# Optimization experiments

Measured on AMD Instinct MI355X. Metric: run time of the kernel, lower is better.

The kernel has to match this reference:

```python
import jax, jax.numpy as jnp
import numpy as np

H = 32  # hidden size per direction (hard-wired in module)


def _gru_scan(x_proj, W_hh, b_hh, reverse):
    """x_proj: [T, B, 3H] = x @ W_ih.T + b_ih (precomputed). Returns all hidden states [T, B, H].
    Gate order follows PyTorch: (r, z, n)."""
    def step(h, xp):
        gh = h @ W_hh.T + b_hh                      # [B, 3H]
        xr, xz, xn = jnp.split(xp, 3, axis=-1)
        hr, hz, hn = jnp.split(gh, 3, axis=-1)
        r = jax.nn.sigmoid(xr + hr)
        z = jax.nn.sigmoid(xz + hz)
        n = jnp.tanh(xn + r * hn)
        h_new = (1.0 - z) * n + z * h
        return h_new, h_new

    B = x_proj.shape[1]
    h0 = jnp.zeros((B, H), x_proj.dtype)
    _, ys = jax.lax.scan(step, h0, x_proj, reverse=reverse)
    return ys  # ys[t] = hidden after consuming x[t] (fwd) or x[T-1..t] (bwd)


def setup_inputs() -> dict:
    key = jax.random.key(0)
    ks = jax.random.split(key, 14)
    B, T = 2048, 512
    s_ih = 1.0 / np.sqrt(H)
    inp = {
        "x": jax.random.normal(ks[0], (B, T, 1), dtype=jnp.float32),
        # forward-direction GRU params (PyTorch layout: [3H, in], [3H, H], [3H])
        "W_ih_f": jax.random.uniform(ks[1], (3 * H, 1), jnp.float32, -s_ih, s_ih),
        "W_hh_f": jax.random.uniform(ks[2], (3 * H, H), jnp.float32, -s_ih, s_ih),
        "b_ih_f": jax.random.uniform(ks[3], (3 * H,), jnp.float32, -s_ih, s_ih),
        "b_hh_f": jax.random.uniform(ks[4], (3 * H,), jnp.float32, -s_ih, s_ih),
        # backward-direction GRU params
        "W_ih_b": jax.random.uniform(ks[5], (3 * H, 1), jnp.float32, -s_ih, s_ih),
        "W_hh_b": jax.random.uniform(ks[6], (3 * H, H), jnp.float32, -s_ih, s_ih),
        "b_ih_b": jax.random.uniform(ks[7], (3 * H,), jnp.float32, -s_ih, s_ih),
        "b_hh_b": jax.random.uniform(ks[8], (3 * H,), jnp.float32, -s_ih, s_ih),
        # MLP head: Linear(64,16) -> ReLU -> Linear(16,1) -> Sigmoid
        "W1": jax.random.uniform(ks[9], (16, 2 * H), jnp.float32, -0.125, 0.125),
        "b1": jax.random.uniform(ks[10], (16,), jnp.float32, -0.125, 0.125),
        "W2": jax.random.uniform(ks[11], (1, 16), jnp.float32, -0.25, 0.25),
        "b2": jax.random.uniform(ks[12], (1,), jnp.float32, -0.25, 0.25),
    }
    return inp


def reference(x, W_ih_f, W_hh_f, b_ih_f, b_hh_f,
              W_ih_b, W_hh_b, b_ih_b, b_hh_b,
              W1, b1, W2, b2):
    xt = jnp.swapaxes(x, 0, 1)                 # [T, B, 1]
    # Precompute input projections for all timesteps (input_size=1 so this is cheap)
    xpf = xt @ W_ih_f.T + b_ih_f               # [T, B, 3H]
    xpb = xt @ W_ih_b.T + b_ih_b               # [T, B, 3H]
    ys_f = _gru_scan(xpf, W_hh_f, b_hh_f, reverse=False)
    ys_b = _gru_scan(xpb, W_hh_b, b_hh_b, reverse=True)
    # out[:, -1, :] in torch = concat(fwd hidden at t=T-1, bwd hidden at t=T-1)
    out_last = jnp.concatenate([ys_f[-1], ys_b[-1]], axis=-1)   # [B, 64]
    h1 = jax.nn.relu(out_last @ W1.T + b1)                      # [B, 16]
    return jax.nn.sigmoid(h1 @ W2.T + b2)                       # [B, 1]
```

## Files before the change

### kernel.cpp

```cpp
#include <hip/hip_runtime.h>


typedef float vf2 __attribute__((ext_vector_type(2)));
typedef float vf4 __attribute__((ext_vector_type(4)));
typedef _Float16 f16;
typedef f16 h2 __attribute__((ext_vector_type(2)));
typedef f16 h8 __attribute__((ext_vector_type(8)));

#define TT 512
#define HH 32

#define PIN(v) asm volatile("" : "+v"(v))

#define LOG2E 1.44269504f

__device__ __forceinline__ float fast_sigm(float a) {
  return __builtin_amdgcn_rcpf(1.0f + __builtin_amdgcn_exp2f(-LOG2E * a));
}
__device__ __forceinline__ float fast_tanh(float a) {
  return __builtin_fmaf(-2.0f,
      __builtin_amdgcn_rcpf(1.0f + __builtin_amdgcn_exp2f(2.0f * LOG2E * a)),
      1.0f);
}

__device__ __forceinline__ h2 pack_h2(vf2 a, float s) {
  h2 r = {(f16)(a.x * s), (f16)(a.y * s)};
  return r;
}

#define LDW16(P, BASE, S) \
  h2 P##0=pack_h2(Wp[(BASE)+0],(S)),  P##1=pack_h2(Wp[(BASE)+1],(S)), \
     P##2=pack_h2(Wp[(BASE)+2],(S)),  P##3=pack_h2(Wp[(BASE)+3],(S)), \
     P##4=pack_h2(Wp[(BASE)+4],(S)),  P##5=pack_h2(Wp[(BASE)+5],(S)), \
     P##6=pack_h2(Wp[(BASE)+6],(S)),  P##7=pack_h2(Wp[(BASE)+7],(S)), \
     P##8=pack_h2(Wp[(BASE)+8],(S)),  P##9=pack_h2(Wp[(BASE)+9],(S)), \
     P##A=pack_h2(Wp[(BASE)+10],(S)), P##B=pack_h2(Wp[(BASE)+11],(S)), \
     P##C=pack_h2(Wp[(BASE)+12],(S)), P##D=pack_h2(Wp[(BASE)+13],(S)), \
     P##E=pack_h2(Wp[(BASE)+14],(S)), P##F=pack_h2(Wp[(BASE)+15],(S)); \
  PIN(P##0);PIN(P##1);PIN(P##2);PIN(P##3);PIN(P##4);PIN(P##5);PIN(P##6);PIN(P##7); \
  PIN(P##8);PIN(P##9);PIN(P##A);PIN(P##B);PIN(P##C);PIN(P##D);PIN(P##E);PIN(P##F)

#define FDOT16(A0, A1, P, SEED) \
  float A0 = __builtin_amdgcn_fdot2(q0, P##0, (SEED), false); \
  float A1 = __builtin_amdgcn_fdot2(q1, P##1, 0.0f, false); \
  A0 = __builtin_amdgcn_fdot2(q2, P##2, A0, false);  A1 = __builtin_amdgcn_fdot2(q3, P##3, A1, false); \
  A0 = __builtin_amdgcn_fdot2(q4, P##4, A0, false);  A1 = __builtin_amdgcn_fdot2(q5, P##5, A1, false); \
  A0 = __builtin_amdgcn_fdot2(q6, P##6, A0, false);  A1 = __builtin_amdgcn_fdot2(q7, P##7, A1, false); \
  A0 = __builtin_amdgcn_fdot2(q8, P##8, A0, false);  A1 = __builtin_amdgcn_fdot2(q9, P##9, A1, false); \
  A0 = __builtin_amdgcn_fdot2(qA, P##A, A0, false);  A1 = __builtin_amdgcn_fdot2(qB, P##B, A1, false); \
  A0 = __builtin_amdgcn_fdot2(qC, P##C, A0, false);  A1 = __builtin_amdgcn_fdot2(qD, P##D, A1, false); \
  A0 = __builtin_amdgcn_fdot2(qE, P##E, A0, false);  A1 = __builtin_amdgcn_fdot2(qF, P##F, A1, false)

__global__ __launch_bounds__(256)
__attribute__((amdgpu_waves_per_eu(1, 1)))
void gru_bidir_head(const float* __restrict__ X,
                    const float* __restrict__ Wih_f, const float* __restrict__ Whh_f,
                    const float* __restrict__ bih_f, const float* __restrict__ bhh_f,
                    const float* __restrict__ Wih_b,
                    const float* __restrict__ bih_b, const float* __restrict__ bhh_b,
                    const float* __restrict__ W1, const float* __restrict__ b1,
                    const float* __restrict__ W2, const float* __restrict__ b2,
                    float* __restrict__ out)
{
  __shared__ float xbuf[8][TT];
  __shared__ f16   hbuf[8][HH];
  __shared__ float obuf[8][64];

  const int g  = threadIdx.x & 31;
  const int rs = threadIdx.x >> 5;
  const int b  = (blockIdx.x << 3) + rs;

  const vf4* Xr4 = (const vf4*)(X + (size_t)b * TT);
  vf4* xb4 = (vf4*)&xbuf[rs][0];
  #pragma unroll
  for (int q = 0; q < 4; ++q) xb4[g + 32 * q] = Xr4[g + 32 * q];

  const vf2* Wp = (const vf2*)Whh_f;
  const float s1 = -LOG2E;
  const float s2 = 2.0f * LOG2E;
  LDW16(Wr, g * 16, s1);
  LDW16(Wz, (HH + g) * 16, s1);
  LDW16(Wn, (2 * HH + g) * 16, s2);

  float xwr = Wih_f[g] * s1, xwz = Wih_f[HH + g] * s1, xwn = Wih_f[2*HH + g] * s2;
  float cbr = (bih_f[g]      + bhh_f[g])      * s1;
  float cbz = (bih_f[HH + g] + bhh_f[HH + g]) * s1;
  float cbn = bih_f[2*HH + g] * s2;
  float cbh = bhh_f[2*HH + g] * s2;
  PIN(xwr); PIN(xwz); PIN(xwn); PIN(cbr); PIN(cbz); PIN(cbn); PIN(cbh);

  float h = 0.0f;
  hbuf[rs][g] = (f16)0.0f;
  __builtin_amdgcn_wave_barrier();

  const h8*  hv = (const h8*)&hbuf[rs][0];
  const vf4* xv = (const vf4*)&xbuf[rs][0];
  vf4 x4 = xv[0];

  #pragma unroll 1
  for (int tg = 0; tg < TT / 4; ++tg) {
    const vf4 x4n = xv[tg + 1 < TT / 4 ? tg + 1 : tg];
    #pragma unroll
    for (int u = 0; u < 4; ++u) {
      const float x = (u == 0) ? x4.x : (u == 1) ? x4.y : (u == 2) ? x4.z : x4.w;

      h8 H0 = hv[0], H1 = hv[1], H2 = hv[2], H3 = hv[3];
      h2 q0 = {H0[0], H0[1]}, q1 = {H0[2], H0[3]}, q2 = {H0[4], H0[5]}, q3 = {H0[6], H0[7]},
         q4 = {H1[0], H1[1]}, q5 = {H1[2], H1[3]}, q6 = {H1[4], H1[5]}, q7 = {H1[6], H1[7]},
         q8 = {H2[0], H2[1]}, q9 = {H2[2], H2[3]}, qA = {H2[4], H2[5]}, qB = {H2[6], H2[7]},
         qC = {H3[0], H3[1]}, qD = {H3[2], H3[3]}, qE = {H3[4], H3[5]}, qF = {H3[6], H3[7]};
      asm volatile("" : "+v"(q0), "+v"(q1), "+v"(q2), "+v"(q3),
                        "+v"(q4), "+v"(q5), "+v"(q6), "+v"(q7),
                        "+v"(q8), "+v"(q9), "+v"(qA), "+v"(qB),
                        "+v"(qC), "+v"(qD), "+v"(qE), "+v"(qF));

      FDOT16(Ra, Rb, Wr, __builtin_fmaf(x, xwr, cbr));
      FDOT16(Za, Zb, Wz, __builtin_fmaf(x, xwz, cbz));
      FDOT16(Na, Nb, Wn, cbh);

      const float ar = Ra + Rb;
      const float az = Za + Zb;
      const float r = __builtin_amdgcn_rcpf(1.0f + __builtin_amdgcn_exp2f(ar));
      const float z = __builtin_amdgcn_rcpf(1.0f + __builtin_amdgcn_exp2f(az));
      const float y = __builtin_fmaf(r, Na + Nb, __builtin_fmaf(x, xwn, cbn));
      const float n = __builtin_fmaf(-2.0f,
          __builtin_amdgcn_rcpf(1.0f + __builtin_amdgcn_exp2f(y)), 1.0f);
      h = __builtin_fmaf(z, h - n, n);

      hbuf[rs][g] = (f16)h;
      __builtin_amdgcn_wave_barrier();
    }
    x4 = x4n;
  }

  const float xl  = xbuf[rs][TT - 1];
  const float rb  = fast_sigm(__builtin_fmaf(xl, Wih_b[g],      bih_b[g]      + bhh_b[g]));
  const float zb  = fast_sigm(__builtin_fmaf(xl, Wih_b[HH + g], bih_b[HH + g] + bhh_b[HH + g]));
  const float xnb = __builtin_fmaf(xl, Wih_b[2*HH + g], bih_b[2*HH + g]);
  const float nb  = fast_tanh(__builtin_fmaf(rb, bhh_b[2*HH + g], xnb));
  const float hb  = nb - zb * nb;

  obuf[rs][g]      = h;
  obuf[rs][32 + g] = hb;
  __builtin_amdgcn_wave_barrier();

  const int j = g & 15;
  const vf4* W1r = (const vf4*)(W1 + j * 64);
  const vf4* hc  = (const vf4*)&obuf[rs][0];
  vf4 a4 = W1r[0] * hc[0];
  #pragma unroll
  for (int q = 1; q < 16; ++q)
    a4 = __builtin_elementwise_fma(W1r[q], hc[q], a4);
  float acc = b1[j] + (a4.x + a4.y) + (a4.z + a4.w);
  float h1 = fmaxf(acc, 0.0f) * W2[j];
  h1 += __shfl_down(h1, 8, 16);
  h1 += __shfl_down(h1, 4, 16);
  h1 += __shfl_down(h1, 2, 16);
  h1 += __shfl_down(h1, 1, 16);
  if (g == 0) out[b] = fast_sigm(h1 + b2[0]);
}

extern "C" void kernel_launch(void* const* d_in, const int* in_sizes, int n_in,
                              void* d_out, int out_size, void* d_ws, size_t ws_size,
                              hipStream_t stream) {
  const float* X     = (const float*)d_in[0];
  const float* Wih_f = (const float*)d_in[1];
  const float* Whh_f = (const float*)d_in[2];
  const float* bih_f = (const float*)d_in[3];
  const float* bhh_f = (const float*)d_in[4];
  const float* Wih_b = (const float*)d_in[5];
  const float* bih_b = (const float*)d_in[7];
  const float* bhh_b = (const float*)d_in[8];
  const float* W1    = (const float*)d_in[9];
  const float* b1    = (const float*)d_in[10];
  const float* W2    = (const float*)d_in[11];
  const float* b2    = (const float*)d_in[12];
  float* out = (float*)d_out;

  gru_bidir_head<<<256, 256, 0, stream>>>(X, Wih_f, Whh_f, bih_f, bhh_f,
                                          Wih_b, bih_b, bhh_b, W1, b1, W2, b2, out);
}
```

Measured before the change: 177.4 us.

## Split GRU hidden-dot reduction across wave halves, one batch row per wave

```diff
diff --git a/kernel.cpp b/kernel.cpp
--- a/kernel.cpp
+++ b/kernel.cpp
@@ -28,31 +28,27 @@
   return r;
 }
 
-#define LDW16(P, BASE, S) \
-  h2 P##0=pack_h2(Wp[(BASE)+0],(S)),  P##1=pack_h2(Wp[(BASE)+1],(S)), \
-     P##2=pack_h2(Wp[(BASE)+2],(S)),  P##3=pack_h2(Wp[(BASE)+3],(S)), \
-     P##4=pack_h2(Wp[(BASE)+4],(S)),  P##5=pack_h2(Wp[(BASE)+5],(S)), \
-     P##6=pack_h2(Wp[(BASE)+6],(S)),  P##7=pack_h2(Wp[(BASE)+7],(S)), \
-     P##8=pack_h2(Wp[(BASE)+8],(S)),  P##9=pack_h2(Wp[(BASE)+9],(S)), \
-     P##A=pack_h2(Wp[(BASE)+10],(S)), P##B=pack_h2(Wp[(BASE)+11],(S)), \
-     P##C=pack_h2(Wp[(BASE)+12],(S)), P##D=pack_h2(Wp[(BASE)+13],(S)), \
-     P##E=pack_h2(Wp[(BASE)+14],(S)), P##F=pack_h2(Wp[(BASE)+15],(S)); \
-  PIN(P##0);PIN(P##1);PIN(P##2);PIN(P##3);PIN(P##4);PIN(P##5);PIN(P##6);PIN(P##7); \
-  PIN(P##8);PIN(P##9);PIN(P##A);PIN(P##B);PIN(P##C);PIN(P##D);PIN(P##E);PIN(P##F)
+#define LDW8(P, BASE, S) \
+  h2 P##0=pack_h2(Wp[(BASE)+0],(S)), P##1=pack_h2(Wp[(BASE)+1],(S)), \
+     P##2=pack_h2(Wp[(BASE)+2],(S)), P##3=pack_h2(Wp[(BASE)+3],(S)), \
+     P##4=pack_h2(Wp[(BASE)+4],(S)), P##5=pack_h2(Wp[(BASE)+5],(S)), \
+     P##6=pack_h2(Wp[(BASE)+6],(S)), P##7=pack_h2(Wp[(BASE)+7],(S)); \
+  PIN(P##0);PIN(P##1);PIN(P##2);PIN(P##3);PIN(P##4);PIN(P##5);PIN(P##6);PIN(P##7)
 
-#define FDOT16(A0, A1, P, SEED) \
-  float A0 = __builtin_amdgcn_fdot2(q0, P##0, (SEED), false); \
-  float A1 = __builtin_amdgcn_fdot2(q1, P##1, 0.0f, false); \
-  A0 = __builtin_amdgcn_fdot2(q2, P##2, A0, false);  A1 = __builtin_amdgcn_fdot2(q3, P##3, A1, false); \
-  A0 = __builtin_amdgcn_fdot2(q4, P##4, A0, false);  A1 = __builtin_amdgcn_fdot2(q5, P##5, A1, false); \
-  A0 = __builtin_amdgcn_fdot2(q6, P##6, A0, false);  A1 = __builtin_amdgcn_fdot2(q7, P##7, A1, false); \
-  A0 = __builtin_amdgcn_fdot2(q8, P##8, A0, false);  A1 = __builtin_amdgcn_fdot2(q9, P##9, A1, false); \
-  A0 = __builtin_amdgcn_fdot2(qA, P##A, A0, false);  A1 = __builtin_amdgcn_fdot2(qB, P##B, A1, false); \
-  A0 = __builtin_amdgcn_fdot2(qC, P##C, A0, false);  A1 = __builtin_amdgcn_fdot2(qD, P##D, A1, false); \
-  A0 = __builtin_amdgcn_fdot2(qE, P##E, A0, false);  A1 = __builtin_amdgcn_fdot2(qF, P##F, A1, false)
+#define FDOT8(RES, P) \
+  float RES; \
+  { float c0 = __builtin_amdgcn_fdot2(q0, P##0, 0.0f, false); \
+    float c1 = __builtin_amdgcn_fdot2(q1, P##1, 0.0f, false); \
+    c0 = __builtin_amdgcn_fdot2(q2, P##2, c0, false); \
+    c1 = __builtin_amdgcn_fdot2(q3, P##3, c1, false); \
+    c0 = __builtin_amdgcn_fdot2(q4, P##4, c0, false); \
+    c1 = __builtin_amdgcn_fdot2(q5, P##5, c1, false); \
+    c0 = __builtin_amdgcn_fdot2(q6, P##6, c0, false); \
+    c1 = __builtin_amdgcn_fdot2(q7, P##7, c1, false); \
+    RES = c0 + c1; }
 
 __global__ __launch_bounds__(256)
-__attribute__((amdgpu_waves_per_eu(1, 1)))
+__attribute__((amdgpu_waves_per_eu(2, 2)))
 void gru_bidir_head(const float* __restrict__ X,
                     const float* __restrict__ Wih_f, const float* __restrict__ Whh_f,
                     const float* __restrict__ bih_f, const float* __restrict__ bhh_f,
@@ -62,39 +58,42 @@
                     const float* __restrict__ W2, const float* __restrict__ b2,
                     float* __restrict__ out)
 {
-  __shared__ float xbuf[8][TT];
-  __shared__ f16   hbuf[8][HH];
-  __shared__ float obuf[8][64];
+  __shared__ float xbuf[4][TT];
+  __shared__ f16   hbuf[4][2][HH];
+  __shared__ float obuf[4][64];
 
-  const int g  = threadIdx.x & 31;
-  const int rs = threadIdx.x >> 5;
-  const int b  = (blockIdx.x << 3) + rs;
+  const int L = threadIdx.x & 63;
+  const int w = threadIdx.x >> 6;
+  const int i = L & 31;
+  const int k = L >> 5;
+  const int b = (blockIdx.x << 2) + w;
 
   const vf4* Xr4 = (const vf4*)(X + (size_t)b * TT);
-  vf4* xb4 = (vf4*)&xbuf[rs][0];
-  #pragma unroll
-  for (int q = 0; q < 4; ++q) xb4[g + 32 * q] = Xr4[g + 32 * q];
+  vf4* xb4 = (vf4*)&xbuf[w][0];
+  xb4[L]      = Xr4[L];
+  xb4[64 + L] = Xr4[64 + L];
 
   const vf2* Wp = (const vf2*)Whh_f;
   const float s1 = -LOG2E;
   const float s2 = 2.0f * LOG2E;
-  LDW16(Wr, g * 16, s1);
-  LDW16(Wz, (HH + g) * 16, s1);
-  LDW16(Wn, (2 * HH + g) * 16, s2);
+  const int hb8 = k * 8;
+  LDW8(Wr, (i)        * 16 + hb8, s1);
+  LDW8(Wz, (HH + i)   * 16 + hb8, s1);
+  LDW8(Wn, (2*HH + i) * 16 + hb8, s2);
 
-  float xwr = Wih_f[g] * s1, xwz = Wih_f[HH + g] * s1, xwn = Wih_f[2*HH + g] * s2;
-  float cbr = (bih_f[g]      + bhh_f[g])      * s1;
-  float cbz = (bih_f[HH + g] + bhh_f[HH + g]) * s1;
-  float cbn = bih_f[2*HH + g] * s2;
-  float cbh = bhh_f[2*HH + g] * s2;
+  float xwr = Wih_f[i] * s1, xwz = Wih_f[HH + i] * s1, xwn = Wih_f[2*HH + i] * s2;
+  float cbr = (bih_f[i]      + bhh_f[i])      * s1;
+  float cbz = (bih_f[HH + i] + bhh_f[HH + i]) * s1;
+  float cbn = bih_f[2*HH + i] * s2;
+  float cbh = bhh_f[2*HH + i] * s2;
   PIN(xwr); PIN(xwz); PIN(xwn); PIN(cbr); PIN(cbz); PIN(cbn); PIN(cbh);
 
   float h = 0.0f;
-  hbuf[rs][g] = (f16)0.0f;
+  hbuf[w][k][i] = (f16)0.0f;
   __builtin_amdgcn_wave_barrier();
 
-  const h8*  hv = (const h8*)&hbuf[rs][0];
-  const vf4* xv = (const vf4*)&xbuf[rs][0];
+  const h8*  hv = (const h8*)&hbuf[w][k][16 * k];
+  const vf4* xv = (const vf4*)&xbuf[w][0];
   vf4 x4 = xv[0];
 
   #pragma unroll 1
@@ -104,49 +103,49 @@
     for (int u = 0; u < 4; ++u) {
       const float x = (u == 0) ? x4.x : (u == 1) ? x4.y : (u == 2) ? x4.z : x4.w;
 
-      h8 H0 = hv[0], H1 = hv[1], H2 = hv[2], H3 = hv[3];
-      h2 q0 = {H0[0], H0[1]}, q1 = {H0[2], H0[3]}, q2 = {H0[4], H0[5]}, q3 = {H0[6], H0[7]},
-         q4 = {H1[0], H1[1]}, q5 = {H1[2], H1[3]}, q6 = {H1[4], H1[5]}, q7 = {H1[6], H1[7]},
-         q8 = {H2[0], H2[1]}, q9 = {H2[2], H2[3]}, qA = {H2[4], H2[5]}, qB = {H2[6], H2[7]},
-         qC = {H3[0], H3[1]}, qD = {H3[2], H3[3]}, qE = {H3[4], H3[5]}, qF = {H3[6], H3[7]};
+      h8 H0 = hv[0], H1 = hv[1];
+      h2 q0 = {H0[0], H0[1]}, q1 = {H0[2], H0[3]},
+         q2 = {H0[4], H0[5]}, q3 = {H0[6], H0[7]},
+         q4 = {H1[0], H1[1]}, q5 = {H1[2], H1[3]},
+         q6 = {H1[4], H1[5]}, q7 = {H1[6], H1[7]};
       asm volatile("" : "+v"(q0), "+v"(q1), "+v"(q2), "+v"(q3),
-                        "+v"(q4), "+v"(q5), "+v"(q6), "+v"(q7),
-                        "+v"(q8), "+v"(q9), "+v"(qA), "+v"(qB),
-                        "+v"(qC), "+v"(qD), "+v"(qE), "+v"(qF));
+                        "+v"(q4), "+v"(q5), "+v"(q6), "+v"(q7));
 
-      FDOT16(Ra, Rb, Wr, __builtin_fmaf(x, xwr, cbr));
-      FDOT16(Za, Zb, Wz, __builtin_fmaf(x, xwz, cbz));
-      FDOT16(Na, Nb, Wn, cbh);
+      FDOT8(pr, Wr);
+      FDOT8(pz, Wz);
+      FDOT8(pn, Wn);
+      pr += __shfl_xor(pr, 32, 64);
+      pz += __shfl_xor(pz, 32, 64);
+      pn += __shfl_xor(pn, 32, 64);
 
-      const float ar = Ra + Rb;
-      const float az = Za + Zb;
+      const float ar = __builtin_fmaf(x, xwr, cbr) + pr;
+      const float az = __builtin_fmaf(x, xwz, cbz) + pz;
       const float r = __builtin_amdgcn_rcpf(1.0f + __builtin_amdgcn_exp2f(ar));
       const float z = __builtin_amdgcn_rcpf(1.0f + __builtin_amdgcn_exp2f(az));
-      const float y = __builtin_fmaf(r, Na + Nb, __builtin_fmaf(x, xwn, cbn));
+      const float y = __builtin_fmaf(r, pn + cbh, __builtin_fmaf(x, xwn, cbn));
       const float n = __builtin_fmaf(-2.0f,
           __builtin_amdgcn_rcpf(1.0f + __builtin_amdgcn_exp2f(y)), 1.0f);
       h = __builtin_fmaf(z, h - n, n);
 
-      hbuf[rs][g] = (f16)h;
+      hbuf[w][k][i] = (f16)h;
       __builtin_amdgcn_wave_barrier();
     }
     x4 = x4n;
   }
 
-  const float xl  = xbuf[rs][TT - 1];
-  const float rb  = fast_sigm(__builtin_fmaf(xl, Wih_b[g],      bih_b[g]      + bhh_b[g]));
-  const float zb  = fast_sigm(__builtin_fmaf(xl, Wih_b[HH + g], bih_b[HH + g] + bhh_b[HH + g]));
-  const float xnb = __builtin_fmaf(xl, Wih_b[2*HH + g], bih_b[2*HH + g]);
-  const float nb  = fast_tanh(__builtin_fmaf(rb, bhh_b[2*HH + g], xnb));
+  const float xl  = xbuf[w][TT - 1];
+  const float rb  = fast_sigm(__builtin_fmaf(xl, Wih_b[i],      bih_b[i]      + bhh_b[i]));
+  const float zb  = fast_sigm(__builtin_fmaf(xl, Wih_b[HH + i], bih_b[HH + i] + bhh_b[HH + i]));
+  const float xnb = __builtin_fmaf(xl, Wih_b[2*HH + i], bih_b[2*HH + i]);
+  const float nb  = fast_tanh(__builtin_fmaf(rb, bhh_b[2*HH + i], xnb));
   const float hb  = nb - zb * nb;
 
-  obuf[rs][g]      = h;
-  obuf[rs][32 + g] = hb;
+  obuf[w][k * 32 + i] = k ? hb : h;
   __builtin_amdgcn_wave_barrier();
 
-  const int j = g & 15;
+  const int j = L & 15;
   const vf4* W1r = (const vf4*)(W1 + j * 64);
-  const vf4* hc  = (const vf4*)&obuf[rs][0];
+  const vf4* hc  = (const vf4*)&obuf[w][0];
   vf4 a4 = W1r[0] * hc[0];
   #pragma unroll
   for (int q = 1; q < 16; ++q)
@@ -157,7 +156,7 @@
   h1 += __shfl_down(h1, 4, 16);
   h1 += __shfl_down(h1, 2, 16);
   h1 += __shfl_down(h1, 1, 16);
-  if (g == 0) out[b] = fast_sigm(h1 + b2[0]);
+  if (L == 0) out[b] = fast_sigm(h1 + b2[0]);
 }
 
 extern "C" void kernel_launch(void* const* d_in, const int* in_sizes, int n_in,
@@ -177,6 +176,6 @@
   const float* b2    = (const float*)d_in[12];
   float* out = (float*)d_out;
 
-  gru_bidir_head<<<256, 256, 0, stream>>>(X, Wih_f, Whh_f, bih_f, bhh_f,
+  gru_bidir_head<<<512, 256, 0, stream>>>(X, Wih_f, Whh_f, bih_f, bhh_f,
                                           Wih_b, bih_b, bhh_b, W1, b1, W2, b2, out);
 }
```

Measured after the change: 224.7 us. 26.6% more time.
